# Kernel tuning notes

Hardware: AMD Instinct MI355X
Metric: run time of the kernel (lower is better)

Reference implementation:

```python
import jax, jax.numpy as jnp
from jax import lax
import numpy as np


def _conv(x, w):
    # x: [B,Cin,H,W], w: [Cout,Cin,kh,kw] -> [B,Cout,H,W], SAME padding
    return lax.conv_general_dilated(x, w, (1, 1), 'SAME')


def setup_inputs() -> dict:
    key = jax.random.key(0)
    ks = jax.random.split(key, 16)
    B, Hh, W = 8, 256, 256
    inputs = jax.random.normal(ks[0], (B, Hh, W), jnp.float32)
    H0 = jax.random.normal(ks[1], (B, Hh, W), jnp.float32)
    C0 = jax.random.normal(ks[2], (B, 2, Hh, W), jnp.float32)
    # learned scalars: c2 ~ U(0,1), sf ~ N(0, 0.01) shifted away from 0 (it is a divisor)
    c2 = jax.random.uniform(ks[3], (1,), jnp.float32, 0.0, 1.0)
    sf = 0.01 * jax.random.normal(ks[4], (1,), jnp.float32) + 0.02
    # RedNet (assumed small conv encoder-decoder): 1->32->64->32->1, 3x3 SAME, ReLU
    w1 = 0.1 * jax.random.normal(ks[5], (32, 1, 3, 3), jnp.float32)
    b1 = jnp.zeros((32,), jnp.float32)
    w2 = 0.1 * jax.random.normal(ks[6], (64, 32, 3, 3), jnp.float32)
    b2 = jnp.zeros((64,), jnp.float32)
    w3 = 0.1 * jax.random.normal(ks[7], (32, 64, 3, 3), jnp.float32)
    b3 = jnp.zeros((32,), jnp.float32)
    w4 = 0.1 * jax.random.normal(ks[8], (1, 32, 3, 3), jnp.float32)
    b4 = jnp.zeros((1,), jnp.float32)
    return dict(inputs=inputs, H0=H0, C0=C0, c2=c2, sf=sf,
                w1=w1, b1=b1, w2=w2, b2=b2, w3=w3, b3=b3, w4=w4, b4=b4)


def reference(inputs, H0, C0, c2, sf, w1, b1, w2, b2, w3, b3, w4, b4):
    # Fixed 5-point Laplacian stencil (non-trainable in the original module)
    lap_k = jnp.array([[0., 1., 0.], [1., -4., 1.], [0., 1., 0.]],
                      dtype=inputs.dtype)[None, None]  # [1,1,3,3]

    # torch chain: C' = permute/matmul(Wcc^T)/permute + wcu*U
    #   reduces exactly to: C'[:,0] = inputs, C'[:,1] = C_old[:,0]
    C_new = jnp.stack([inputs, C0[:, 0]], axis=1)  # [B,2,H,W]

    V = inputs - H0  # [B,H,W]

    # H = whc . C' = 2*C'[:,0] - C'[:,1] = 2*inputs - C_old[:,0]
    lap = _conv(inputs[:, None], lap_k)[:, 0]  # [B,H,W]
    H = 2.0 * inputs - C0[:, 0] + c2 * lap

    # RedNet on scaled residual V
    h = (V / sf)[:, None]  # [B,1,H,W]
    h = jax.nn.relu(_conv(h, w1) + b1[None, :, None, None])
    h = jax.nn.relu(_conv(h, w2) + b2[None, :, None, None])
    h = jax.nn.relu(_conv(h, w3) + b3[None, :, None, None])
    V_hat = (_conv(h, w4) + b4[None, :, None, None])[:, 0] * sf  # [B,H,W]

    outputs = H + V_hat
    return (outputs, H, C_new, V, V_hat)
```

## Files before the change

### kernel.cpp

```cpp
#include <hip/hip_runtime.h>

#define PLANE 65536
#define WIDTH 256
#define PADW 258
#define PADPLANE 66564

typedef __bf16 v8bf __attribute__((ext_vector_type(8)));
typedef float  v4f  __attribute__((ext_vector_type(4)));

typedef const __attribute__((address_space(1))) unsigned int* gas_ptr;
typedef __attribute__((address_space(3))) unsigned int* las_ptr;

__device__ __forceinline__ void gl_lds(const void* g, void* l) {
  __builtin_amdgcn_global_load_lds((gas_ptr)g, (las_ptr)l, 16, 0, 0);
}

__device__ __forceinline__ int swz(int c) {
  return (c & ~7) | ((c & 7) ^ ((c >> 3) & 7));
}

__device__ __forceinline__ unsigned int pack2(float a, float b) {
  __bf16 ba = (__bf16)a, bb = (__bf16)b;
  unsigned short sa = __builtin_bit_cast(unsigned short, ba);
  unsigned short sb = __builtin_bit_cast(unsigned short, bb);
  return (unsigned int)sa | ((unsigned int)sb << 16);
}

#define WT_N 37440
#define ZR_N (8 * 1028 * 64)
__global__ __launch_bounds__(256) void wz_k(
    const float* __restrict__ w1, const float* __restrict__ w2,
    const float* __restrict__ w3, const float* __restrict__ w4,
    float* __restrict__ w1t, __bf16* __restrict__ B2t,
    __bf16* __restrict__ B3t, float* __restrict__ w4t,
    __bf16* __restrict__ a1, __bf16* __restrict__ a2,
    __bf16* __restrict__ a3)
{
  int t = blockIdx.x * 256 + threadIdx.x;
  if (t < WT_N) {
    if (t < 288) {
      int tap = t >> 5, cout = t & 31;
      w1t[t] = w1[cout * 9 + tap];
    }
    int t2 = t - 288;
    if (t2 >= 0 && t2 < 18432) {
      int cout = t2 / 288, k = t2 % 288;
      int tap = k / 32, cin = k % 32;
      B2t[t2] = (__bf16)w2[cout * 288 + cin * 9 + tap];
    }
    int t3 = t - (288 + 18432);
    if (t3 >= 0 && t3 < 18432) {
      int cout = t3 / 576, k = t3 % 576;
      int tap = k / 64, cin = k % 64;
      B3t[t3] = (__bf16)w3[cout * 576 + cin * 9 + tap];
    }
    int t4 = t - (288 + 18432 + 18432);
    if (t4 >= 0 && t4 < 288) {
      int tap = t4 >> 5, cin = t4 & 31;
      w4t[t4] = w4[cin * 9 + tap];
    }
    return;
  }
  int idx = t - WT_N;
  if (idx >= ZR_N) return;
  unsigned int* p; int C2;
  const int R1 = 8 * 1028 * 16, R2 = 8 * 1028 * 32;
  if (idx < R1)           { p = (unsigned int*)a1; C2 = 16; }
  else if (idx < R1 + R2) { p = (unsigned int*)a2; C2 = 32; idx -= R1; }
  else                    { p = (unsigned int*)a3; C2 = 16; idx -= R1 + R2; }
  int ch = idx % C2;
  int pr = idx / C2;
  int b = pr / 1028, r = pr % 1028;
  int y, x;
  if      (r < 258) { y = 0;           x = r; }
  else if (r < 516) { y = 257;         x = r - 258; }
  else if (r < 772) { y = r - 516 + 1; x = 0; }
  else              { y = r - 772 + 1; x = 257; }
  p[((size_t)b * PADPLANE + y * PADW + x) * C2 + ch] = 0;
}

__global__ __launch_bounds__(256) void prepconv1_k(
    const float* __restrict__ inputs, const float* __restrict__ H0,
    const float* __restrict__ C0, const float* __restrict__ c2p,
    const float* __restrict__ sfp, const float* __restrict__ w1t,
    const float* __restrict__ b1, float* __restrict__ dout,
    __bf16* __restrict__ act1)
{
  const int x = threadIdx.x, y = blockIdx.x, b = blockIdx.y;
  const int p = b * PLANE + y * WIDTH + x;
  const float c2 = c2p[0], sf = sfp[0], rsf = 1.0f / sf;

  float iv[3][3], hv[3][3];
  #pragma unroll
  for (int dy = 0; dy < 3; dy++) {
    int yy = y + dy - 1;
    #pragma unroll
    for (int dx = 0; dx < 3; dx++) {
      int xx = x + dx - 1;
      bool ok = (yy >= 0 && yy < 256 && xx >= 0 && xx < 256);
      int pn = p + (dy - 1) * WIDTH + (dx - 1);
      iv[dy][dx] = ok ? inputs[pn] : 0.f;
      hv[dy][dx] = ok ? H0[pn]     : 0.f;
    }
  }
  const float in = iv[1][1], h0 = hv[1][1];
  const float c0a = C0[b * 131072 + y * WIDTH + x];
  float lap = iv[0][1] + iv[2][1] + iv[1][0] + iv[1][2] - 4.f * in;
  float Hv = 2.f * in - c0a + c2 * lap;
  float V  = in - h0;
  dout[524288 + p]  = Hv;
  dout[2097152 + p] = V;
  dout[1048576 + b * 131072 + y * WIDTH + x]         = in;
  dout[1048576 + b * 131072 + 65536 + y * WIDTH + x] = c0a;

  float acc[32];
  #pragma unroll
  for (int i = 0; i < 32; i++) acc[i] = b1[i];
  #pragma unroll
  for (int tap = 0; tap < 9; tap++) {
    float v = (iv[tap / 3][tap % 3] - hv[tap / 3][tap % 3]) * rsf;
    const float* wp = w1t + tap * 32;
    #pragma unroll
    for (int i = 0; i < 32; i++) acc[i] = fmaf(wp[i], v, acc[i]);
  }
  unsigned int u[16];
  #pragma unroll
  for (int j = 0; j < 16; j++)
    u[j] = pack2(fmaxf(acc[2*j], 0.f), fmaxf(acc[2*j+1], 0.f));
  size_t pa = ((size_t)b * PADPLANE + (y+1) * PADW + (x+1)) * 32;
  uint4* op = reinterpret_cast<uint4*>(act1 + pa);
  #pragma unroll
  for (int j = 0; j < 4; j++)
    op[j] = make_uint4(u[4*j], u[4*j+1], u[4*j+2], u[4*j+3]);
}

#define C2ROWB 8320
template<int ROWS>
__global__ __launch_bounds__(256, 2) void conv2_k(
    const __bf16* __restrict__ in, const __bf16* __restrict__ Bt,
    const float* __restrict__ bias, __bf16* __restrict__ out)
{
  const int lane = threadIdx.x & 63, wave = threadIdx.x >> 6;
  const int l15 = lane & 15, q = lane >> 4;
  const int y0 = blockIdx.x * ROWS, xt = blockIdx.y, b = blockIdx.z;
  const int x0 = xt * 128;
  __shared__ __align__(16) char smem[4 * C2ROWB];
  const __bf16* plane = in + (size_t)b * PADPLANE * 32;

  auto stage = [&](int pr, char* lrow) {
    const char* g = (const char*)(plane + ((size_t)pr * PADW + x0) * 32);
    const int base = wave * 130;
    #pragma unroll
    for (int j = 0; j < 2; j++) {
      int c = base + j * 64 + lane;
      gl_lds(g + (size_t)swz(c) * 16, lrow + (base + j * 64) * 16);
    }
    if (lane < 2) {
      int c = base + 128 + lane;
      gl_lds(g + (size_t)swz(c) * 16, lrow + (base + 128) * 16);
    }
  };

  v8bf breg[9][4];
  #pragma unroll
  for (int tap = 0; tap < 9; tap++)
    #pragma unroll
    for (int nt = 0; nt < 4; nt++)
      breg[tap][nt] = *(const v8bf*)(Bt + (size_t)(nt * 16 + l15) * 288
                                        + tap * 32 + q * 8);
  float bv[4];
  #pragma unroll
  for (int nt = 0; nt < 4; nt++) bv[nt] = bias[nt * 16 + l15];

  #pragma unroll
  for (int r = 0; r < 3; r++) stage(y0 + r, smem + r * C2ROWB);
  asm volatile("s_waitcnt vmcnt(0)" ::: "memory");
  __builtin_amdgcn_s_barrier();
  __builtin_amdgcn_sched_barrier(0);

  for (int i = 0; i < ROWS; i++) {
    if (i + 3 < ROWS + 2)
      stage(y0 + i + 3, smem + ((i + 3) & 3) * C2ROWB);

    v4f acc[2][4];
    #pragma unroll
    for (int mt = 0; mt < 2; mt++)
      #pragma unroll
      for (int nt = 0; nt < 4; nt++)
        acc[mt][nt] = (v4f){bv[nt], bv[nt], bv[nt], bv[nt]};

    __builtin_amdgcn_s_setprio(1);
    #pragma unroll
    for (int tap = 0; tap < 9; tap++) {
      const int dy = tap / 3, dx = tap % 3;
      const char* srow = smem + ((i + dy) & 3) * C2ROWB;
      v8bf af[2];
      #pragma unroll
      for (int mt = 0; mt < 2; mt++) {
        int P = wave * 32 + mt * 16 + l15 + dx;
        af[mt] = *(const v8bf*)(srow + (size_t)swz(P * 4 + q) * 16);
      }
      #pragma unroll
      for (int mt = 0; mt < 2; mt++)
        #pragma unroll
        for (int nt = 0; nt < 4; nt++)
          acc[mt][nt] = __builtin_amdgcn_mfma_f32_16x16x32_bf16(
              af[mt], breg[tap][nt], acc[mt][nt], 0, 0, 0);
    }
    __builtin_amdgcn_s_setprio(0);
    {
      size_t rb = ((size_t)b * PADPLANE + (size_t)(y0 + i + 1) * PADW
                   + x0 + 1) * 64;
      #pragma unroll
      for (int mt = 0; mt < 2; mt++) {
        #pragma unroll
        for (int r = 0; r < 4; r++) {
          size_t pa = rb + (size_t)(wave * 32 + mt * 16 + q * 4 + r) * 64;
          #pragma unroll
          for (int nt = 0; nt < 4; nt++)
            out[pa + nt * 16 + l15] = (__bf16)fmaxf(acc[mt][nt][r], 0.f);
        }
      }
    }
    asm volatile("s_waitcnt vmcnt(24)" ::: "memory");
    __builtin_amdgcn_s_barrier();
    __builtin_amdgcn_sched_barrier(0);
  }
}

#define C3ROWB 8448
template<int ROWS>
__global__ __launch_bounds__(256, 2) void conv3_k(
    const __bf16* __restrict__ in, const __bf16* __restrict__ Bt,
    const float* __restrict__ bias, __bf16* __restrict__ out)
{
  const int lane = threadIdx.x & 63, wave = threadIdx.x >> 6;
  const int l15 = lane & 15, q = lane >> 4;
  const int y0 = blockIdx.x * ROWS, xt = blockIdx.y, b = blockIdx.z;
  const int x0 = xt * 64;
  __shared__ __align__(16) char smem[8 * C3ROWB];
  const __bf16* plane = in + (size_t)b * PADPLANE * 64;

  auto stage = [&](int pr, char* lrow) {
    const char* g = (const char*)(plane + ((size_t)pr * PADW + x0) * 64);
    const int base = wave * 132;
    #pragma unroll
    for (int j = 0; j < 2; j++) {
      int c = base + j * 64 + lane;
      gl_lds(g + (size_t)swz(c) * 16, lrow + (base + j * 64) * 16);
    }
    if (lane < 4) {
      int c = base + 128 + lane;
      gl_lds(g + (size_t)swz(c) * 16, lrow + (base + 128) * 16);
    }
  };

  v8bf breg[9][2][2];
  #pragma unroll
  for (int tap = 0; tap < 9; tap++)
    #pragma unroll
    for (int kb = 0; kb < 2; kb++)
      #pragma unroll
      for (int nt = 0; nt < 2; nt++)
        breg[tap][kb][nt] = *(const v8bf*)(Bt + (size_t)(nt * 16 + l15) * 576
                                              + tap * 64 + kb * 32 + q * 8);
  float bv[2] = {bias[l15], bias[16 + l15]};

  #pragma unroll
  for (int r = 0; r < 4; r++) stage(y0 + r, smem + r * C3ROWB);
  asm volatile("s_waitcnt vmcnt(0)" ::: "memory");
  __builtin_amdgcn_s_barrier();
  __builtin_amdgcn_sched_barrier(0);

  for (int ps = 0; ps < ROWS / 2; ps++) {
    if (2 * ps + 4 < ROWS + 2)
      stage(y0 + 2 * ps + 4, smem + ((2 * ps + 4) & 7) * C3ROWB);
    if (2 * ps + 5 < ROWS + 2)
      stage(y0 + 2 * ps + 5, smem + ((2 * ps + 5) & 7) * C3ROWB);

    v4f acc[2][2];
    #pragma unroll
    for (int rr = 0; rr < 2; rr++)
      #pragma unroll
      for (int nt = 0; nt < 2; nt++)
        acc[rr][nt] = (v4f){bv[nt], bv[nt], bv[nt], bv[nt]};

    __builtin_amdgcn_s_setprio(1);
    #pragma unroll
    for (int t = 0; t < 4; t++) {
      const char* srow = smem + ((2 * ps + t) & 7) * C3ROWB;
      #pragma unroll
      for (int dx = 0; dx < 3; dx++) {
        #pragma unroll
        for (int kb = 0; kb < 2; kb++) {
          int P = wave * 16 + l15 + dx;
          v8bf af = *(const v8bf*)(srow + (size_t)swz(P * 8 + kb * 4 + q) * 16);
          #pragma unroll
          for (int nt = 0; nt < 2; nt++) {
            if (t <= 2)
              acc[0][nt] = __builtin_amdgcn_mfma_f32_16x16x32_bf16(
                  af, breg[t * 3 + dx][kb][nt], acc[0][nt], 0, 0, 0);
            if (t >= 1)
              acc[1][nt] = __builtin_amdgcn_mfma_f32_16x16x32_bf16(
                  af, breg[(t - 1) * 3 + dx][kb][nt], acc[1][nt], 0, 0, 0);
          }
        }
      }
    }
    __builtin_amdgcn_s_setprio(0);
    {
      #pragma unroll
      for (int rr = 0; rr < 2; rr++) {
        size_t rb = ((size_t)b * PADPLANE
                     + (size_t)(y0 + 2 * ps + rr + 1) * PADW + x0 + 1) * 32;
        #pragma unroll
        for (int r = 0; r < 4; r++) {
          size_t pa = rb + (size_t)(wave * 16 + q * 4 + r) * 32;
          #pragma unroll
          for (int nt = 0; nt < 2; nt++)
            out[pa + nt * 16 + l15] = (__bf16)fmaxf(acc[rr][nt][r], 0.f);
        }
      }
    }
    asm volatile("s_waitcnt vmcnt(12)" ::: "memory");
    __builtin_amdgcn_s_barrier();
    __builtin_amdgcn_sched_barrier(0);
  }
}

#define C4ROWB 16512
__global__ __launch_bounds__(256, 2) void conv4_k(
    const __bf16* __restrict__ act3, const float* __restrict__ w4t,
    const float* __restrict__ b4, const float* __restrict__ sfp,
    float* __restrict__ dout)
{
  const int x = threadIdx.x, lane = threadIdx.x & 63, wave = threadIdx.x >> 6;
  const int y0 = blockIdx.x * 2, b = blockIdx.y;
  const float b4v = b4[0], sf = sfp[0];
  const __bf16* plane = act3 + (size_t)b * PADPLANE * 32;
  __shared__ __align__(16) char smem[4 * C4ROWB];

  #pragma unroll
  for (int r = 0; r < 4; r++) {
    const char* g = (const char*)(plane + (size_t)(y0 + r) * PADW * 32);
    char* lrow = smem + r * C4ROWB;
    #pragma unroll
    for (int k = 0; k < 4; k++) {
      int c = k * 256 + wave * 64 + lane;
      gl_lds(g + (size_t)swz(c) * 16, lrow + (k * 256 + wave * 64) * 16);
    }
    if (wave == 0 && lane < 8) {
      int c = 1024 + lane;
      gl_lds(g + (size_t)swz(c) * 16, lrow + 1024 * 16);
    }
  }
  asm volatile("s_waitcnt vmcnt(0)" ::: "memory");
  __builtin_amdgcn_s_barrier();

  float acc0 = b4v, acc1 = b4v;
  #pragma unroll
  for (int t = 0; t < 4; t++) {
    const char* srow = smem + t * C4ROWB;
    uint4 L[12];
    #pragma unroll
    for (int j = 0; j < 12; j++) {
      int chunk = (x + (j >> 2)) * 4 + (j & 3);
      L[j] = *(const uint4*)(srow + (size_t)swz(chunk) * 16);
    }
    #pragma unroll
    for (int j = 0; j < 12; j++) {
      const int dx = j >> 2, c0 = (j & 3) * 8;
      unsigned int uu[4] = {L[j].x, L[j].y, L[j].z, L[j].w};
      float f[8];
      #pragma unroll
      for (int k = 0; k < 4; k++) {
        f[2*k]   = __builtin_bit_cast(float, uu[k] << 16);
        f[2*k+1] = __builtin_bit_cast(float, uu[k] & 0xFFFF0000u);
      }
      if (t <= 2) {
        const float* wp = w4t + (t * 3 + dx) * 32 + c0;
        #pragma unroll
        for (int k = 0; k < 8; k++) acc0 = fmaf(wp[k], f[k], acc0);
      }
      if (t >= 1) {
        const float* wp = w4t + ((t - 1) * 3 + dx) * 32 + c0;
        #pragma unroll
        for (int k = 0; k < 8; k++) acc1 = fmaf(wp[k], f[k], acc1);
      }
    }
  }
  size_t p0 = ((size_t)b << 16) + (size_t)y0 * WIDTH + x;
  float vh0 = acc0 * sf, vh1 = acc1 * sf;
  dout[p0]                   = dout[524288 + p0] + vh0;
  dout[2621440 + p0]         = vh0;
  dout[p0 + WIDTH]           = dout[524288 + p0 + WIDTH] + vh1;
  dout[2621440 + p0 + WIDTH] = vh1;
}

extern "C" void kernel_launch(void* const* d_in, const int* in_sizes, int n_in,
                              void* d_out, int out_size, void* d_ws, size_t ws_size,
                              hipStream_t stream) {
  const float* inputs = (const float*)d_in[0];
  const float* H0     = (const float*)d_in[1];
  const float* C0     = (const float*)d_in[2];
  const float* c2     = (const float*)d_in[3];
  const float* sf     = (const float*)d_in[4];
  const float* w1     = (const float*)d_in[5];
  const float* b1     = (const float*)d_in[6];
  const float* w2     = (const float*)d_in[7];
  const float* b2     = (const float*)d_in[8];
  const float* w3     = (const float*)d_in[9];
  const float* b3     = (const float*)d_in[10];
  const float* w4     = (const float*)d_in[11];
  const float* b4     = (const float*)d_in[12];
  float* out = (float*)d_out;
  float* ws  = (float*)d_ws;

  float*  w1t  = ws;
  float*  w4t  = ws + 288;
  __bf16* B2t  = (__bf16*)(ws + 576);
  __bf16* B3t  = (__bf16*)(ws + 9792);
  __bf16* act1 = (__bf16*)(ws + 19008);
  __bf16* act2 = act1 + (size_t)8 * PADPLANE * 32;
  __bf16* act3 = act2 + (size_t)8 * PADPLANE * 64;

  wz_k<<<2203, 256, 0, stream>>>(w1, w2, w3, w4, w1t, B2t, B3t, w4t,
                                 act1, act2, act3);
  prepconv1_k<<<dim3(256, 8), 256, 0, stream>>>(inputs, H0, C0, c2, sf,
                                                w1t, b1, out, act1);
  conv2_k<8><<<dim3(32, 2, 8), 256, 0, stream>>>(act1, B2t, b2, act2);
  conv3_k<8><<<dim3(32, 4, 8), 256, 0, stream>>>(act2, B3t, b3, act3);
  conv4_k<<<dim3(128, 8), 256, 0, stream>>>(act3, w4t, b4, sf, out);
}
```

Before: 175.0 us.

## Fuse conv2 and conv3 into one kernel keeping act2 in shared memory

```diff
diff --git a/kernel.cpp b/kernel.cpp
--- a/kernel.cpp
+++ b/kernel.cpp
@@ -18,6 +18,8 @@
 __device__ __forceinline__ int swz(int c) {
   return (c & ~7) | ((c & 7) ^ ((c >> 3) & 7));
 }
+
+__device__ __forceinline__ int m6(int x) { return x >= 6 ? x - 6 : x; }
 
 __device__ __forceinline__ unsigned int pack2(float a, float b) {
   __bf16 ba = (__bf16)a, bb = (__bf16)b;
@@ -27,14 +29,13 @@
 }
 
 #define WT_N 37440
-#define ZR_N (8 * 1028 * 64)
+#define ZR_N (8 * 1028 * 32)
 __global__ __launch_bounds__(256) void wz_k(
     const float* __restrict__ w1, const float* __restrict__ w2,
     const float* __restrict__ w3, const float* __restrict__ w4,
     float* __restrict__ w1t, __bf16* __restrict__ B2t,
     __bf16* __restrict__ B3t, float* __restrict__ w4t,
-    __bf16* __restrict__ a1, __bf16* __restrict__ a2,
-    __bf16* __restrict__ a3)
+    __bf16* __restrict__ a1, __bf16* __restrict__ a3)
 {
   int t = blockIdx.x * 256 + threadIdx.x;
   if (t < WT_N) {
@@ -63,20 +64,19 @@
   }
   int idx = t - WT_N;
   if (idx >= ZR_N) return;
-  unsigned int* p; int C2;
-  const int R1 = 8 * 1028 * 16, R2 = 8 * 1028 * 32;
-  if (idx < R1)           { p = (unsigned int*)a1; C2 = 16; }
-  else if (idx < R1 + R2) { p = (unsigned int*)a2; C2 = 32; idx -= R1; }
-  else                    { p = (unsigned int*)a3; C2 = 16; idx -= R1 + R2; }
-  int ch = idx % C2;
-  int pr = idx / C2;
+  unsigned int* p;
+  const int R1 = 8 * 1028 * 16;
+  if (idx < R1) p = (unsigned int*)a1;
+  else         { p = (unsigned int*)a3; idx -= R1; }
+  int ch = idx & 15;
+  int pr = idx >> 4;
   int b = pr / 1028, r = pr % 1028;
   int y, x;
   if      (r < 258) { y = 0;           x = r; }
   else if (r < 516) { y = 257;         x = r - 258; }
   else if (r < 772) { y = r - 516 + 1; x = 0; }
   else              { y = r - 772 + 1; x = 257; }
-  p[((size_t)b * PADPLANE + y * PADW + x) * C2 + ch] = 0;
+  p[((size_t)b * PADPLANE + y * PADW + x) * 16 + ch] = 0;
 }
 
 __global__ __launch_bounds__(256) void prepconv1_k(
@@ -134,197 +134,175 @@
     op[j] = make_uint4(u[4*j], u[4*j+1], u[4*j+2], u[4*j+3]);
 }
 
-#define C2ROWB 8320
-template<int ROWS>
-__global__ __launch_bounds__(256, 2) void conv2_k(
-    const __bf16* __restrict__ in, const __bf16* __restrict__ Bt,
-    const float* __restrict__ bias, __bf16* __restrict__ out)
+#define A1ROWB 4352
+#define A2ROWB 8448
+__global__ __launch_bounds__(256, 2) void conv23_k(
+    const __bf16* __restrict__ act1, const __bf16* __restrict__ B2t,
+    const float* __restrict__ b2, const __bf16* __restrict__ B3t,
+    const float* __restrict__ b3, __bf16* __restrict__ act3)
 {
   const int lane = threadIdx.x & 63, wave = threadIdx.x >> 6;
   const int l15 = lane & 15, q = lane >> 4;
-  const int y0 = blockIdx.x * ROWS, xt = blockIdx.y, b = blockIdx.z;
-  const int x0 = xt * 128;
-  __shared__ __align__(16) char smem[4 * C2ROWB];
-  const __bf16* plane = in + (size_t)b * PADPLANE * 32;
-
-  auto stage = [&](int pr, char* lrow) {
-    const char* g = (const char*)(plane + ((size_t)pr * PADW + x0) * 32);
-    const int base = wave * 130;
-    #pragma unroll
-    for (int j = 0; j < 2; j++) {
-      int c = base + j * 64 + lane;
-      gl_lds(g + (size_t)swz(c) * 16, lrow + (base + j * 64) * 16);
-    }
-    if (lane < 2) {
-      int c = base + 128 + lane;
-      gl_lds(g + (size_t)swz(c) * 16, lrow + (base + 128) * 16);
-    }
+  const int y0 = blockIdx.x * 8, xt = blockIdx.y, b = blockIdx.z;
+  const int x0 = xt * 64;
+  __shared__ __align__(16) char smem[6 * A2ROWB + 6 * A1ROWB + 1024];
+  char* a2r = smem;
+  char* a1r = smem + 6 * A2ROWB;
+  const __bf16* plane = act1 + (size_t)b * PADPLANE * 32;
+
+  auto stageA1 = [&](int k, int slot) {
+    int a = y0 - 1 + k;
+    a = a < 0 ? 0 : (a > 257 ? 257 : a);
+    const char* g = (const char*)(plane + ((size_t)a * PADW + x0 - 1) * 32);
+    char* lrow = a1r + slot * A1ROWB;
+    const int base = wave * 68;
+    gl_lds(g + (size_t)swz(base + lane) * 16, lrow + base * 16);
+    if (lane < 4)
+      gl_lds(g + (size_t)swz(base + 64 + lane) * 16, lrow + (base + 64) * 16);
   };
 
-  v8bf breg[9][4];
+  v8bf breg2[9];
   #pragma unroll
   for (int tap = 0; tap < 9; tap++)
-    #pragma unroll
-    for (int nt = 0; nt < 4; nt++)
-      breg[tap][nt] = *(const v8bf*)(Bt + (size_t)(nt * 16 + l15) * 288
-                                        + tap * 32 + q * 8);
-  float bv[4];
-  #pragma unroll
-  for (int nt = 0; nt < 4; nt++) bv[nt] = bias[nt * 16 + l15];
-
-  #pragma unroll
-  for (int r = 0; r < 3; r++) stage(y0 + r, smem + r * C2ROWB);
+    breg2[tap] = *(const v8bf*)(B2t + (size_t)(wave * 16 + l15) * 288
+                                    + tap * 32 + q * 8);
+  const float bv2 = b2[wave * 16 + l15];
+
+  const int Mh = wave >> 1, ntw = wave & 1;
+  v8bf breg3[9][2];
+  #pragma unroll
+  for (int tap = 0; tap < 9; tap++)
+    #pragma unroll
+    for (int kb = 0; kb < 2; kb++)
+      breg3[tap][kb] = *(const v8bf*)(B3t + (size_t)(ntw * 16 + l15) * 576
+                                          + tap * 64 + kb * 32 + q * 8);
+  const float bv3 = b3[ntw * 16 + l15];
+
+  auto produce = [&](int t, int s) {
+    char* drow = a2r + s * A2ROWB;
+    int pr = y0 + t;
+    if (pr == 0 || pr == 257) {
+      int c = threadIdx.x;
+      *(uint4*)(drow + (size_t)c * 16)         = make_uint4(0,0,0,0);
+      *(uint4*)(drow + (size_t)(c + 256) * 16) = make_uint4(0,0,0,0);
+      if (c < 16)
+        *(uint4*)(drow + (size_t)(c + 512) * 16) = make_uint4(0,0,0,0);
+      return;
+    }
+    v4f acc[5];
+    #pragma unroll
+    for (int m = 0; m < 5; m++) acc[m] = (v4f){bv2, bv2, bv2, bv2};
+    #pragma unroll
+    for (int tap = 0; tap < 9; tap++) {
+      const int dy = tap / 3, dx = tap % 3;
+      const char* srow = a1r + m6(s + dy) * A1ROWB;
+      #pragma unroll
+      for (int m = 0; m < 5; m++) {
+        int j = m * 16 + l15 + dx;
+        v8bf af = *(const v8bf*)(srow + (size_t)swz(j * 4 + q) * 16);
+        acc[m] = __builtin_amdgcn_mfma_f32_16x16x32_bf16(
+            af, breg2[tap], acc[m], 0, 0, 0);
+      }
+    }
+    const int ch = wave * 16 + l15;
+    const int chunkoff = ch >> 3, byteoff = (ch & 7) * 2;
+    #pragma unroll
+    for (int m = 0; m < 5; m++) {
+      #pragma unroll
+      for (int r = 0; r < 4; r++) {
+        int i = m * 16 + q * 4 + r;
+        bool w = (m < 4) || (q == 0 && r < 2);
+        if (x0 == 0   && i == 0)  w = false;
+        if (x0 == 192 && i == 65) w = false;
+        if (w) {
+          __bf16 v = (__bf16)fmaxf(acc[m][r], 0.f);
+          *(__bf16*)(drow + (size_t)swz(i * 8 + chunkoff) * 16 + byteoff) = v;
+        }
+      }
+    }
+    if (x0 == 0 && threadIdx.x < 8)
+      *(uint4*)(drow + (size_t)swz(threadIdx.x) * 16) = make_uint4(0,0,0,0);
+    if (x0 == 192 && threadIdx.x < 8)
+      *(uint4*)(drow + (size_t)swz(520 + threadIdx.x) * 16) = make_uint4(0,0,0,0);
+  };
+
+  #pragma unroll
+  for (int k = 0; k < 6; k++) stageA1(k, k);
   asm volatile("s_waitcnt vmcnt(0)" ::: "memory");
   __builtin_amdgcn_s_barrier();
   __builtin_amdgcn_sched_barrier(0);
-
-  for (int i = 0; i < ROWS; i++) {
-    if (i + 3 < ROWS + 2)
-      stage(y0 + i + 3, smem + ((i + 3) & 3) * C2ROWB);
-
-    v4f acc[2][4];
-    #pragma unroll
-    for (int mt = 0; mt < 2; mt++)
-      #pragma unroll
-      for (int nt = 0; nt < 4; nt++)
-        acc[mt][nt] = (v4f){bv[nt], bv[nt], bv[nt], bv[nt]};
-
-    __builtin_amdgcn_s_setprio(1);
-    #pragma unroll
-    for (int tap = 0; tap < 9; tap++) {
-      const int dy = tap / 3, dx = tap % 3;
-      const char* srow = smem + ((i + dy) & 3) * C2ROWB;
-      v8bf af[2];
-      #pragma unroll
-      for (int mt = 0; mt < 2; mt++) {
-        int P = wave * 32 + mt * 16 + l15 + dx;
-        af[mt] = *(const v8bf*)(srow + (size_t)swz(P * 4 + q) * 16);
-      }
-      #pragma unroll
-      for (int mt = 0; mt < 2; mt++)
-        #pragma unroll
-        for (int nt = 0; nt < 4; nt++)
-          acc[mt][nt] = __builtin_amdgcn_mfma_f32_16x16x32_bf16(
-              af[mt], breg[tap][nt], acc[mt][nt], 0, 0, 0);
-    }
-    __builtin_amdgcn_s_setprio(0);
-    {
-      size_t rb = ((size_t)b * PADPLANE + (size_t)(y0 + i + 1) * PADW
-                   + x0 + 1) * 64;
-      #pragma unroll
-      for (int mt = 0; mt < 2; mt++) {
-        #pragma unroll
-        for (int r = 0; r < 4; r++) {
-          size_t pa = rb + (size_t)(wave * 32 + mt * 16 + q * 4 + r) * 64;
-          #pragma unroll
-          for (int nt = 0; nt < 4; nt++)
-            out[pa + nt * 16 + l15] = (__bf16)fmaxf(acc[mt][nt][r], 0.f);
-        }
-      }
-    }
-    asm volatile("s_waitcnt vmcnt(24)" ::: "memory");
+  produce(0, 0);
+  produce(1, 1);
+  asm volatile("s_waitcnt lgkmcnt(0)" ::: "memory");
+  __builtin_amdgcn_s_barrier();
+  __builtin_amdgcn_sched_barrier(0);
+
+  int sb = 0;
+  for (int ps = 0; ps < 4; ps++) {
+    if (2 * ps + 6 <= 11) stageA1(2 * ps + 6, sb);
+    if (2 * ps + 7 <= 11) stageA1(2 * ps + 7, m6(sb + 1));
+
+    produce(2 * ps + 2, m6(sb + 2));
+    produce(2 * ps + 3, m6(sb + 3));
+    asm volatile("s_waitcnt lgkmcnt(0)" ::: "memory");
     __builtin_amdgcn_s_barrier();
     __builtin_amdgcn_sched_barrier(0);
-  }
-}
-
-#define C3ROWB 8448
-template<int ROWS>
-__global__ __launch_bounds__(256, 2) void conv3_k(
-    const __bf16* __restrict__ in, const __bf16* __restrict__ Bt,
-    const float* __restrict__ bias, __bf16* __restrict__ out)
-{
-  const int lane = threadIdx.x & 63, wave = threadIdx.x >> 6;
-  const int l15 = lane & 15, q = lane >> 4;
-  const int y0 = blockIdx.x * ROWS, xt = blockIdx.y, b = blockIdx.z;
-  const int x0 = xt * 64;
-  __shared__ __align__(16) char smem[8 * C3ROWB];
-  const __bf16* plane = in + (size_t)b * PADPLANE * 64;
-
-  auto stage = [&](int pr, char* lrow) {
-    const char* g = (const char*)(plane + ((size_t)pr * PADW + x0) * 64);
-    const int base = wave * 132;
-    #pragma unroll
-    for (int j = 0; j < 2; j++) {
-      int c = base + j * 64 + lane;
-      gl_lds(g + (size_t)swz(c) * 16, lrow + (base + j * 64) * 16);
-    }
-    if (lane < 4) {
-      int c = base + 128 + lane;
-      gl_lds(g + (size_t)swz(c) * 16, lrow + (base + 128) * 16);
-    }
-  };
-
-  v8bf breg[9][2][2];
-  #pragma unroll
-  for (int tap = 0; tap < 9; tap++)
-    #pragma unroll
-    for (int kb = 0; kb < 2; kb++)
-      #pragma unroll
-      for (int nt = 0; nt < 2; nt++)
-        breg[tap][kb][nt] = *(const v8bf*)(Bt + (size_t)(nt * 16 + l15) * 576
-                                              + tap * 64 + kb * 32 + q * 8);
-  float bv[2] = {bias[l15], bias[16 + l15]};
-
-  #pragma unroll
-  for (int r = 0; r < 4; r++) stage(y0 + r, smem + r * C3ROWB);
-  asm volatile("s_waitcnt vmcnt(0)" ::: "memory");
-  __builtin_amdgcn_s_barrier();
-  __builtin_amdgcn_sched_barrier(0);
-
-  for (int ps = 0; ps < ROWS / 2; ps++) {
-    if (2 * ps + 4 < ROWS + 2)
-      stage(y0 + 2 * ps + 4, smem + ((2 * ps + 4) & 7) * C3ROWB);
-    if (2 * ps + 5 < ROWS + 2)
-      stage(y0 + 2 * ps + 5, smem + ((2 * ps + 5) & 7) * C3ROWB);
-
-    v4f acc[2][2];
-    #pragma unroll
-    for (int rr = 0; rr < 2; rr++)
-      #pragma unroll
-      for (int nt = 0; nt < 2; nt++)
-        acc[rr][nt] = (v4f){bv[nt], bv[nt], bv[nt], bv[nt]};
-
-    __builtin_amdgcn_s_setprio(1);
-    #pragma unroll
-    for (int t = 0; t < 4; t++) {
-      const char* srow = smem + ((2 * ps + t) & 7) * C3ROWB;
-      #pragma unroll
-      for (int dx = 0; dx < 3; dx++) {
+
+    {
+      v4f acc3[2][2];
+      #pragma unroll
+      for (int rr = 0; rr < 2; rr++)
         #pragma unroll
-        for (int kb = 0; kb < 2; kb++) {
-          int P = wave * 16 + l15 + dx;
-          v8bf af = *(const v8bf*)(srow + (size_t)swz(P * 8 + kb * 4 + q) * 16);
+        for (int mt = 0; mt < 2; mt++)
+          acc3[rr][mt] = (v4f){bv3, bv3, bv3, bv3};
+
+      __builtin_amdgcn_s_setprio(1);
+      #pragma unroll
+      for (int t = 0; t < 4; t++) {
+        const char* srow = a2r + m6(sb + t) * A2ROWB;
+        #pragma unroll
+        for (int dx = 0; dx < 3; dx++) {
           #pragma unroll
-          for (int nt = 0; nt < 2; nt++) {
-            if (t <= 2)
-              acc[0][nt] = __builtin_amdgcn_mfma_f32_16x16x32_bf16(
-                  af, breg[t * 3 + dx][kb][nt], acc[0][nt], 0, 0, 0);
-            if (t >= 1)
-              acc[1][nt] = __builtin_amdgcn_mfma_f32_16x16x32_bf16(
-                  af, breg[(t - 1) * 3 + dx][kb][nt], acc[1][nt], 0, 0, 0);
+          for (int kb = 0; kb < 2; kb++) {
+            v8bf af[2];
+            #pragma unroll
+            for (int mt = 0; mt < 2; mt++) {
+              int P = Mh * 32 + mt * 16 + l15 + dx;
+              af[mt] = *(const v8bf*)(srow + (size_t)swz(P * 8 + kb * 4 + q) * 16);
+            }
+            #pragma unroll
+            for (int mt = 0; mt < 2; mt++) {
+              if (t <= 2)
+                acc3[0][mt] = __builtin_amdgcn_mfma_f32_16x16x32_bf16(
+                    af[mt], breg3[t * 3 + dx][kb], acc3[0][mt], 0, 0, 0);
+              if (t >= 1)
+                acc3[1][mt] = __builtin_amdgcn_mfma_f32_16x16x32_bf16(
+                    af[mt], breg3[(t - 1) * 3 + dx][kb], acc3[1][mt], 0, 0, 0);
+            }
           }
         }
       }
-    }
-    __builtin_amdgcn_s_setprio(0);
-    {
+      __builtin_amdgcn_s_setprio(0);
+
       #pragma unroll
       for (int rr = 0; rr < 2; rr++) {
         size_t rb = ((size_t)b * PADPLANE
                      + (size_t)(y0 + 2 * ps + rr + 1) * PADW + x0 + 1) * 32;
         #pragma unroll
-        for (int r = 0; r < 4; r++) {
-          size_t pa = rb + (size_t)(wave * 16 + q * 4 + r) * 32;
+        for (int mt = 0; mt < 2; mt++) {
           #pragma unroll
-          for (int nt = 0; nt < 2; nt++)
-            out[pa + nt * 16 + l15] = (__bf16)fmaxf(acc[rr][nt][r], 0.f);
+          for (int r = 0; r < 4; r++) {
+            int px = Mh * 32 + mt * 16 + q * 4 + r;
+            act3[rb + (size_t)px * 32 + ntw * 16 + l15] =
+                (__bf16)fmaxf(acc3[rr][mt][r], 0.f);
+          }
         }
       }
     }
-    asm volatile("s_waitcnt vmcnt(12)" ::: "memory");
+    asm volatile("s_waitcnt vmcnt(16)" ::: "memory");
     __builtin_amdgcn_s_barrier();
     __builtin_amdgcn_sched_barrier(0);
+    sb = m6(sb + 2);
   }
 }
 
@@ -421,14 +399,12 @@
   __bf16* B2t  = (__bf16*)(ws + 576);
   __bf16* B3t  = (__bf16*)(ws + 9792);
   __bf16* act1 = (__bf16*)(ws + 19008);
-  __bf16* act2 = act1 + (size_t)8 * PADPLANE * 32;
-  __bf16* act3 = act2 + (size_t)8 * PADPLANE * 64;
-
-  wz_k<<<2203, 256, 0, stream>>>(w1, w2, w3, w4, w1t, B2t, B3t, w4t,
-                                 act1, act2, act3);
+  __bf16* act3 = act1 + (size_t)8 * PADPLANE * 32;
+
+  wz_k<<<1175, 256, 0, stream>>>(w1, w2, w3, w4, w1t, B2t, B3t, w4t,
+                                 act1, act3);
   prepconv1_k<<<dim3(256, 8), 256, 0, stream>>>(inputs, H0, C0, c2, sf,
                                                 w1t, b1, out, act1);
-  conv2_k<8><<<dim3(32, 2, 8), 256, 0, stream>>>(act1, B2t, b2, act2);
-  conv3_k<8><<<dim3(32, 4, 8), 256, 0, stream>>>(act2, B3t, b3, act3);
+  conv23_k<<<dim3(32, 4, 8), 256, 0, stream>>>(act1, B2t, b2, B3t, b3, act3);
   conv4_k<<<dim3(128, 8), 256, 0, stream>>>(act3, w4t, b4, sf, out);
 }
```

New measurement: 178.9 us. +2.2%, slower.
